# Performance work log

Measured on AMD Instinct MI355X. Metric: run time of the kernel, lower is better.

The kernel has to match this reference:

```python
import jax, jax.numpy as jnp
import numpy as np

BN_EPS = 1e-5

def conv1x1(x, w, b):
    # x: [b,c,h,w], w: [o,c], b: [o] -> [b,o,h,w]
    return jnp.einsum('bchw,oc->bohw', x, w) + b[None, :, None, None]

def setup_inputs() -> dict:
    key = jax.random.key(0)
    ks = jax.random.split(key, 12)
    C, Ci = 256, 128  # in_channels, inter_channels (ratio=2)
    B, H, W = 4, 56, 56
    s = 1.0 / np.sqrt(C)
    si = 1.0 / np.sqrt(Ci)
    return {
        'x':       jax.random.normal(ks[0], (B, C, H, W), jnp.float32),
        'w_theta': jax.random.normal(ks[1], (Ci, C), jnp.float32) * s,
        'b_theta': jax.random.normal(ks[2], (Ci,), jnp.float32) * s,
        'w_phi':   jax.random.normal(ks[3], (Ci, C), jnp.float32) * s,
        'b_phi':   jax.random.normal(ks[4], (Ci,), jnp.float32) * s,
        'w_g':     jax.random.normal(ks[5], (Ci, C), jnp.float32) * s,
        'b_g':     jax.random.normal(ks[6], (Ci,), jnp.float32) * s,
        'w_rec':   jax.random.normal(ks[7], (C, Ci), jnp.float32) * si,
        'b_rec':   jax.random.normal(ks[8], (C,), jnp.float32) * si,
        'bn_gamma': jax.random.normal(ks[9], (C,), jnp.float32) * 0.1 + 1.0,
        'bn_beta':  jax.random.normal(ks[10], (C,), jnp.float32) * 0.1,
        'bn_mean':  jax.random.normal(ks[11], (C,), jnp.float32) * 0.1,
        'bn_var':   jnp.ones((C,), jnp.float32),
    }

def reference(x, w_theta, b_theta, w_phi, b_phi, w_g, b_g,
              w_rec, b_rec, bn_gamma, bn_beta, bn_mean, bn_var):
    b, _, h, w = x.shape
    n = h * w
    c = w_theta.shape[0]  # inter_channels
    theta_x = conv1x1(x, w_theta, b_theta).reshape(b, c, n).transpose(0, 2, 1)  # [b,n,c]
    phi_x   = conv1x1(x, w_phi, b_phi).reshape(b, c, n)                         # [b,c,n]
    g_x     = conv1x1(x, w_g, b_g).reshape(b, c, n).transpose(0, 2, 1)          # [b,n,c]
    attention = jnp.matmul(theta_x, phi_x) / n                                  # [b,n,n]
    out = jnp.matmul(attention, g_x).transpose(0, 2, 1).reshape(b, c, h, w)
    out = conv1x1(out, w_rec, b_rec)
    # BatchNorm2d in inference form with given stats
    inv = bn_gamma / jnp.sqrt(bn_var + BN_EPS)
    out = out * inv[None, :, None, None] + (bn_beta - bn_mean * inv)[None, :, None, None]
    return out + x
```

## Files before the change

kernel.cpp:

```cpp
#include <hip/hip_runtime.h>

#define B 4
#define C 256
#define CI 128
#define NPIX 3136
#define KSPLIT 7
#define BN_EPS_F 1e-5f

typedef float f4 __attribute__((ext_vector_type(4)));

__global__ __launch_bounds__(64) void rowsum_kernel(const float* __restrict__ x,
                                                    float* __restrict__ s) {
    int b = blockIdx.y, c = blockIdx.x;
    const float* row = x + ((size_t)(b * C + c)) * NPIX;
    float acc = 0.f;
    for (int n = threadIdx.x; n < NPIX; n += 64) acc += row[n];
#pragma unroll
    for (int off = 32; off > 0; off >>= 1) acc += __shfl_down(acc, off, 64);
    if (threadIdx.x == 0) s[b * C + c] = acc;
}

__global__ __launch_bounds__(256) void xxt_kernel(const float* __restrict__ x,
                                                  float* __restrict__ Gp) {
    int j0 = blockIdx.x * 64, i0 = blockIdx.y * 64;
    int z = blockIdx.z;
    int b = z / KSPLIT, ks = z % KSPLIT;
    __shared__ float xi[64][68];
    __shared__ float xj[64][68];
    int tid = threadIdx.x;
    int tx = tid & 15, ty = tid >> 4;
    float acc[4][4] = {};
    const float* xb = x + (size_t)b * C * NPIX;
    for (int t = 0; t < KSPLIT; ++t) {
        int k0 = (ks * KSPLIT + t) * 64;
        __syncthreads();
#pragma unroll
        for (int l = 0; l < 4; ++l) {
            int idx = tid + l * 256;
            int r = idx >> 4, c4 = (idx & 15) << 2;
            *(f4*)&xi[r][c4] = *(const f4*)&xb[(size_t)(i0 + r) * NPIX + k0 + c4];
            *(f4*)&xj[r][c4] = *(const f4*)&xb[(size_t)(j0 + r) * NPIX + k0 + c4];
        }
        __syncthreads();
        for (int kk = 0; kk < 64; kk += 4) {
            f4 a[4], bb[4];
#pragma unroll
            for (int ii = 0; ii < 4; ++ii) a[ii] = *(const f4*)&xi[ty + 16 * ii][kk];
#pragma unroll
            for (int jj = 0; jj < 4; ++jj) bb[jj] = *(const f4*)&xj[tx + 16 * jj][kk];
#pragma unroll
            for (int q = 0; q < 4; ++q)
#pragma unroll
                for (int ii = 0; ii < 4; ++ii)
#pragma unroll
                    for (int jj = 0; jj < 4; ++jj)
                        acc[ii][jj] += a[ii][q] * bb[jj][q];
        }
    }
    float* Gb = Gp + ((size_t)(ks * B + b)) * C * C;
#pragma unroll
    for (int ii = 0; ii < 4; ++ii)
#pragma unroll
        for (int jj = 0; jj < 4; ++jj)
            Gb[(i0 + ty + 16 * ii) * C + (j0 + tx + 16 * jj)] = acc[ii][jj];
}

__global__ __launch_bounds__(256) void greduce_kernel(const float* __restrict__ Gp,
                                                      float* __restrict__ G) {
    int gid = blockIdx.x * 256 + threadIdx.x;
    float acc = 0.f;
#pragma unroll
    for (int ks = 0; ks < KSPLIT; ++ks) acc += Gp[(size_t)ks * (B * C * C) + gid];
    G[gid] = acc;
}

__global__ __launch_bounds__(256) void uv_kernel(const float* __restrict__ wphi,
                                                 const float* __restrict__ wg,
                                                 const float* __restrict__ s,
                                                 float* __restrict__ u,
                                                 float* __restrict__ v) {
    int b = blockIdx.x;
    __shared__ float sl[C];
    for (int i = threadIdx.x; i < C; i += 256) sl[i] = s[b * C + i];
    __syncthreads();
    int t = threadIdx.x;
    const float* wrow = (t < CI) ? (wphi + t * C) : (wg + (t - CI) * C);
    float acc = 0.f;
    for (int c = 0; c < C; ++c) acc += wrow[c] * sl[c];
    if (t < CI) u[b * CI + t] = acc;
    else        v[b * CI + (t - CI)] = acc;
}

__global__ __launch_bounds__(256) void pmat_kernel(const float* __restrict__ wphi,
                                                   const float* __restrict__ G,
                                                   float* __restrict__ P) {
    int gid = blockIdx.x * 256 + threadIdx.x;
    int b = gid >> 15;
    int i = (gid >> 8) & 127;
    int j = gid & 255;
    const float* wr = wphi + i * C;
    const float* Gb = G + (size_t)b * C * C;
    float acc = 0.f;
    for (int c = 0; c < C; ++c) acc += wr[c] * Gb[c * C + j];
    P[gid] = acc;
}

__global__ __launch_bounds__(256) void mmat_kernel(const float* __restrict__ P,
                                                   const float* __restrict__ wg,
                                                   const float* __restrict__ u,
                                                   const float* __restrict__ v,
                                                   const float* __restrict__ bphi,
                                                   const float* __restrict__ bg,
                                                   float* __restrict__ M) {
    int gid = blockIdx.x * 256 + threadIdx.x;
    int b = gid >> 14;
    int i = (gid >> 7) & 127;
    int j = gid & 127;
    const float* Pr = P + ((size_t)b * CI + i) * C;
    const float* wr = wg + j * C;
    float acc = 0.f;
    for (int c = 0; c < C; ++c) acc += Pr[c] * wr[c];
    const float invN = 1.0f / (float)NPIX;
    M[gid] = invN * (acc + u[b * CI + i] * bg[j] + bphi[i] * v[b * CI + j])
             + bphi[i] * bg[j];
}

__global__ __launch_bounds__(256) void amat_kernel(const float* __restrict__ wrec,
                                                   const float* __restrict__ M,
                                                   float* __restrict__ A) {
    int gid = blockIdx.x * 256 + threadIdx.x;
    int b = gid >> 15;
    int o = (gid >> 7) & 255;
    int i = gid & 127;
    const float* wr = wrec + o * CI;
    const float* Mb = M + (size_t)b * CI * CI;
    float acc = 0.f;
    for (int j = 0; j < CI; ++j) acc += wr[j] * Mb[i * CI + j];
    A[gid] = acc;
}

__global__ __launch_bounds__(256) void bias_kernel(const float* __restrict__ A,
                                                   const float* __restrict__ btheta,
                                                   const float* __restrict__ brec,
                                                   const float* __restrict__ gamma,
                                                   const float* __restrict__ beta,
                                                   const float* __restrict__ mean,
                                                   const float* __restrict__ var,
                                                   float* __restrict__ bias5) {
    int b = blockIdx.x, o = threadIdx.x;
    const float* Ar = A + ((size_t)b * C + o) * CI;
    float acc = 0.f;
    for (int i = 0; i < CI; ++i) acc += Ar[i] * btheta[i];
    float inv = gamma[o] * rsqrtf(var[o] + BN_EPS_F);
    bias5[b * C + o] = inv * (acc + brec[o]) + beta[o] - mean[o] * inv;
}

__global__ __launch_bounds__(256) void w5_kernel(const float* __restrict__ A,
                                                 const float* __restrict__ wtheta,
                                                 const float* __restrict__ gamma,
                                                 const float* __restrict__ var,
                                                 float* __restrict__ W5) {
    int gid = blockIdx.x * 256 + threadIdx.x;
    int b = gid >> 16;
    int o = (gid >> 8) & 255;
    int c = gid & 255;
    const float* Ar = A + ((size_t)b * C + o) * CI;
    float acc = 0.f;
    for (int i = 0; i < CI; ++i) acc += Ar[i] * wtheta[i * C + c];
    float inv = gamma[o] * rsqrtf(var[o] + BN_EPS_F);
    W5[gid] = inv * acc;
}

__global__ __launch_bounds__(256) void final_kernel(const float* __restrict__ x,
                                                    const float* __restrict__ W5,
                                                    const float* __restrict__ bias5,
                                                    float* __restrict__ out) {
    int b = blockIdx.z;
    int o0 = blockIdx.y * 64, n0 = blockIdx.x * 64;
    __shared__ float wl[64][68];
    __shared__ float xl[64][68];
    int tid = threadIdx.x;
    int tx = tid & 15, ty = tid >> 4;
    float acc[4][4] = {};
    const float* W5b = W5 + (size_t)b * C * C;
    const float* xb = x + (size_t)b * C * NPIX;
    for (int k0 = 0; k0 < C; k0 += 64) {
        __syncthreads();
#pragma unroll
        for (int l = 0; l < 4; ++l) {
            int idx = tid + l * 256;
            int r = idx >> 4, c4 = (idx & 15) << 2;
            *(f4*)&wl[r][c4] = *(const f4*)&W5b[(o0 + r) * C + k0 + c4];
            *(f4*)&xl[r][c4] = *(const f4*)&xb[(size_t)(k0 + r) * NPIX + n0 + c4];
        }
        __syncthreads();
        for (int kk = 0; kk < 64; kk += 4) {
            f4 a[4], bb[4];
#pragma unroll
            for (int i = 0; i < 4; ++i) a[i] = *(const f4*)&wl[ty + 16 * i][kk];
#pragma unroll
            for (int q = 0; q < 4; ++q) bb[q] = *(const f4*)&xl[kk + q][tx * 4];
#pragma unroll
            for (int q = 0; q < 4; ++q)
#pragma unroll
                for (int i = 0; i < 4; ++i)
#pragma unroll
                    for (int j = 0; j < 4; ++j)
                        acc[i][j] += a[i][q] * bb[q][j];
        }
    }
#pragma unroll
    for (int i = 0; i < 4; ++i) {
        int o = o0 + ty + 16 * i;
        float bias = bias5[b * C + o];
        int n = n0 + tx * 4;
        const f4 xr = *(const f4*)&xb[(size_t)o * NPIX + n];
        f4 r;
#pragma unroll
        for (int j = 0; j < 4; ++j) r[j] = acc[i][j] + bias + xr[j];
        *(f4*)&out[((size_t)b * C + o) * NPIX + n] = r;
    }
}

extern "C" void kernel_launch(void* const* d_in, const int* in_sizes, int n_in,
                              void* d_out, int out_size, void* d_ws, size_t ws_size,
                              hipStream_t stream) {
    const float* x       = (const float*)d_in[0];
    const float* w_theta = (const float*)d_in[1];
    const float* b_theta = (const float*)d_in[2];
    const float* w_phi   = (const float*)d_in[3];
    const float* b_phi   = (const float*)d_in[4];
    const float* w_g     = (const float*)d_in[5];
    const float* b_g     = (const float*)d_in[6];
    const float* w_rec   = (const float*)d_in[7];
    const float* b_rec   = (const float*)d_in[8];
    const float* gamma   = (const float*)d_in[9];
    const float* beta    = (const float*)d_in[10];
    const float* mean    = (const float*)d_in[11];
    const float* var     = (const float*)d_in[12];
    float* out = (float*)d_out;

    float* Gp    = out;
    float* G     = out + 1835008;
    float* P     = out + 2097152;
    float* M     = out + 2228224;
    float* A     = out + 2293760;
    float* ws    = (float*)d_ws;
    float* s     = ws;
    float* u     = ws + 1024;
    float* v     = ws + 1536;
    float* bias5 = ws + 2048;
    float* W5    = ws + 3072;

    rowsum_kernel<<<dim3(C, B), dim3(64), 0, stream>>>(x, s);
    xxt_kernel<<<dim3(4, 4, B * KSPLIT), dim3(256), 0, stream>>>(x, Gp);
    greduce_kernel<<<dim3(B * C * C / 256), dim3(256), 0, stream>>>(Gp, G);
    uv_kernel<<<dim3(B), dim3(256), 0, stream>>>(w_phi, w_g, s, u, v);
    pmat_kernel<<<dim3(B * CI * C / 256), dim3(256), 0, stream>>>(w_phi, G, P);
    mmat_kernel<<<dim3(B * CI * CI / 256), dim3(256), 0, stream>>>(P, w_g, u, v, b_phi, b_g, M);
    amat_kernel<<<dim3(B * C * CI / 256), dim3(256), 0, stream>>>(w_rec, M, A);
    bias_kernel<<<dim3(B), dim3(256), 0, stream>>>(A, b_theta, b_rec, gamma, beta, mean, var, bias5);
    w5_kernel<<<dim3(B * C * C / 256), dim3(256), 0, stream>>>(A, w_theta, gamma, var, W5);
    final_kernel<<<dim3(NPIX / 64, C / 64, B), dim3(256), 0, stream>>>(x, W5, bias5, out);
}
```

Measured before the change: 148.3 us.

## Use bf16 MFMA for the Gram and final GEMMs with a pre-converted copy of x

Adds a prep kernel that converts x to bf16 and also writes a transposed [n, c] bf16 copy. The x·xᵀ Gram kernel and the final W5·x kernel are rewritten to use mfma_f32_16x16x32_bf16, loading operands straight from global memory instead of staging them in shared memory. W5 is now stored in bf16. This swaps the FP32 FMA loops for matrix-core throughput, at the cost of an extra conversion pass over x, reduced precision, and epilogue stores that are no longer vectorised.

```diff
diff --git a/kernel.cpp b/kernel.cpp
--- a/kernel.cpp
+++ b/kernel.cpp
@@ -4,10 +4,19 @@
 #define C 256
 #define CI 128
 #define NPIX 3136
-#define KSPLIT 7
+#define KS 7
 #define BN_EPS_F 1e-5f
 
 typedef float f4 __attribute__((ext_vector_type(4)));
+typedef float f32x4 __attribute__((ext_vector_type(4)));
+typedef short short8 __attribute__((ext_vector_type(8)));
+typedef short short4v __attribute__((ext_vector_type(4)));
+
+__device__ inline short f2bf(float f) {
+    unsigned u = __builtin_bit_cast(unsigned, f);
+    unsigned r = (u + 0x7FFFu + ((u >> 16) & 1u)) >> 16;
+    return (short)r;
+}
 
 __global__ __launch_bounds__(64) void rowsum_kernel(const float* __restrict__ x,
                                                     float* __restrict__ s) {
@@ -20,49 +29,69 @@
     if (threadIdx.x == 0) s[b * C + c] = acc;
 }
 
-__global__ __launch_bounds__(256) void xxt_kernel(const float* __restrict__ x,
-                                                  float* __restrict__ Gp) {
-    int j0 = blockIdx.x * 64, i0 = blockIdx.y * 64;
+__global__ __launch_bounds__(256) void prep_kernel(const float* __restrict__ x,
+                                                   short* __restrict__ xbf,
+                                                   short* __restrict__ xT) {
+    int b = blockIdx.z, c0 = blockIdx.y * 64, n0 = blockIdx.x * 64;
+    __shared__ short lds[64][65];
+    int t = threadIdx.x;
+    int nf = (t & 15) * 4;
+    int cr = t >> 4;
+#pragma unroll
+    for (int it = 0; it < 4; ++it) {
+        int c = cr + 16 * it;
+        f4 v = *(const f4*)&x[((size_t)(b * C + c0 + c)) * NPIX + n0 + nf];
+        short4v s4;
+#pragma unroll
+        for (int i = 0; i < 4; ++i) s4[i] = f2bf(v[i]);
+        *(short4v*)&xbf[((size_t)(b * C + c0 + c)) * NPIX + n0 + nf] = s4;
+#pragma unroll
+        for (int i = 0; i < 4; ++i) lds[nf + i][c] = s4[i];
+    }
+    __syncthreads();
+#pragma unroll
+    for (int it = 0; it < 4; ++it) {
+        int n = cr + 16 * it;
+        short4v s4;
+#pragma unroll
+        for (int i = 0; i < 4; ++i) s4[i] = lds[n][nf + i];
+        *(short4v*)&xT[((size_t)b * NPIX + n0 + n) * C + c0 + nf] = s4;
+    }
+}
+
+__global__ __launch_bounds__(256) void xxt_mfma(const short* __restrict__ xbf,
+                                                float* __restrict__ Gp) {
     int z = blockIdx.z;
-    int b = z / KSPLIT, ks = z % KSPLIT;
-    __shared__ float xi[64][68];
-    __shared__ float xj[64][68];
-    int tid = threadIdx.x;
-    int tx = tid & 15, ty = tid >> 4;
-    float acc[4][4] = {};
-    const float* xb = x + (size_t)b * C * NPIX;
-    for (int t = 0; t < KSPLIT; ++t) {
-        int k0 = (ks * KSPLIT + t) * 64;
-        __syncthreads();
-#pragma unroll
-        for (int l = 0; l < 4; ++l) {
-            int idx = tid + l * 256;
-            int r = idx >> 4, c4 = (idx & 15) << 2;
-            *(f4*)&xi[r][c4] = *(const f4*)&xb[(size_t)(i0 + r) * NPIX + k0 + c4];
-            *(f4*)&xj[r][c4] = *(const f4*)&xb[(size_t)(j0 + r) * NPIX + k0 + c4];
-        }
-        __syncthreads();
-        for (int kk = 0; kk < 64; kk += 4) {
-            f4 a[4], bb[4];
-#pragma unroll
-            for (int ii = 0; ii < 4; ++ii) a[ii] = *(const f4*)&xi[ty + 16 * ii][kk];
-#pragma unroll
-            for (int jj = 0; jj < 4; ++jj) bb[jj] = *(const f4*)&xj[tx + 16 * jj][kk];
-#pragma unroll
-            for (int q = 0; q < 4; ++q)
-#pragma unroll
-                for (int ii = 0; ii < 4; ++ii)
-#pragma unroll
-                    for (int jj = 0; jj < 4; ++jj)
-                        acc[ii][jj] += a[ii][q] * bb[jj][q];
-        }
-    }
-    float* Gb = Gp + ((size_t)(ks * B + b)) * C * C;
-#pragma unroll
-    for (int ii = 0; ii < 4; ++ii)
-#pragma unroll
-        for (int jj = 0; jj < 4; ++jj)
-            Gb[(i0 + ty + 16 * ii) * C + (j0 + tx + 16 * jj)] = acc[ii][jj];
+    int b = z / KS, ks = z % KS;
+    int tid = threadIdx.x, lane = tid & 63, wid = tid >> 6;
+    int ibase = blockIdx.y * 128 + (wid >> 1) * 64;
+    int jbase = blockIdx.x * 128 + (wid & 1) * 64;
+    int lm = lane & 15, lk = (lane >> 4) * 8;
+    const short* A0 = xbf + ((size_t)(b * C) + ibase + lm) * NPIX + lk;
+    const short* B0 = xbf + ((size_t)(b * C) + jbase + lm) * NPIX + lk;
+    f32x4 acc[4][4] = {};
+    int kend = ks * 448 + 448;
+    for (int k = ks * 448; k < kend; k += 32) {
+        short8 a[4], bv[4];
+#pragma unroll
+        for (int mi = 0; mi < 4; ++mi) a[mi] = *(const short8*)(A0 + (size_t)mi * 16 * NPIX + k);
+#pragma unroll
+        for (int nj = 0; nj < 4; ++nj) bv[nj] = *(const short8*)(B0 + (size_t)nj * 16 * NPIX + k);
+#pragma unroll
+        for (int mi = 0; mi < 4; ++mi)
+#pragma unroll
+            for (int nj = 0; nj < 4; ++nj)
+                acc[mi][nj] = __builtin_amdgcn_mfma_f32_16x16x32_bf16(a[mi], bv[nj], acc[mi][nj], 0, 0, 0);
+    }
+    float* out = Gp + ((size_t)(ks * B + b)) * C * C;
+    int r0 = (lane >> 4) * 4;
+#pragma unroll
+    for (int mi = 0; mi < 4; ++mi)
+#pragma unroll
+        for (int r = 0; r < 4; ++r)
+#pragma unroll
+            for (int nj = 0; nj < 4; ++nj)
+                out[(ibase + mi * 16 + r0 + r) * C + jbase + nj * 16 + lm] = acc[mi][nj][r];
 }
 
 __global__ __launch_bounds__(256) void greduce_kernel(const float* __restrict__ Gp,
@@ -70,7 +99,7 @@
     int gid = blockIdx.x * 256 + threadIdx.x;
     float acc = 0.f;
 #pragma unroll
-    for (int ks = 0; ks < KSPLIT; ++ks) acc += Gp[(size_t)ks * (B * C * C) + gid];
+    for (int ks = 0; ks < KS; ++ks) acc += Gp[(size_t)ks * (B * C * C) + gid];
     G[gid] = acc;
 }
 
@@ -159,7 +188,7 @@
                                                  const float* __restrict__ wtheta,
                                                  const float* __restrict__ gamma,
                                                  const float* __restrict__ var,
-                                                 float* __restrict__ W5) {
+                                                 short* __restrict__ W5bf) {
     int gid = blockIdx.x * 256 + threadIdx.x;
     int b = gid >> 16;
     int o = (gid >> 8) & 255;
@@ -168,57 +197,50 @@
     float acc = 0.f;
     for (int i = 0; i < CI; ++i) acc += Ar[i] * wtheta[i * C + c];
     float inv = gamma[o] * rsqrtf(var[o] + BN_EPS_F);
-    W5[gid] = inv * acc;
-}
-
-__global__ __launch_bounds__(256) void final_kernel(const float* __restrict__ x,
-                                                    const float* __restrict__ W5,
-                                                    const float* __restrict__ bias5,
-                                                    float* __restrict__ out) {
-    int b = blockIdx.z;
-    int o0 = blockIdx.y * 64, n0 = blockIdx.x * 64;
-    __shared__ float wl[64][68];
-    __shared__ float xl[64][68];
-    int tid = threadIdx.x;
-    int tx = tid & 15, ty = tid >> 4;
-    float acc[4][4] = {};
-    const float* W5b = W5 + (size_t)b * C * C;
-    const float* xb = x + (size_t)b * C * NPIX;
-    for (int k0 = 0; k0 < C; k0 += 64) {
-        __syncthreads();
-#pragma unroll
-        for (int l = 0; l < 4; ++l) {
-            int idx = tid + l * 256;
-            int r = idx >> 4, c4 = (idx & 15) << 2;
-            *(f4*)&wl[r][c4] = *(const f4*)&W5b[(o0 + r) * C + k0 + c4];
-            *(f4*)&xl[r][c4] = *(const f4*)&xb[(size_t)(k0 + r) * NPIX + n0 + c4];
+    W5bf[gid] = f2bf(inv * acc);
+}
+
+__global__ __launch_bounds__(256) void final_mfma(const float* __restrict__ x,
+                                                  const short* __restrict__ W5bf,
+                                                  const short* __restrict__ xT,
+                                                  const float* __restrict__ bias5,
+                                                  float* __restrict__ out) {
+    int b = blockIdx.y;
+    int n0 = blockIdx.x * 64;
+    int tid = threadIdx.x, lane = tid & 63, wid = tid >> 6;
+    int obase = wid * 64;
+    int lm = lane & 15, lk = (lane >> 4) * 8;
+    const short* A0 = W5bf + ((size_t)(b * C) + obase + lm) * C + lk;
+    const short* B0 = xT + ((size_t)b * NPIX + n0 + lm) * C + lk;
+    f32x4 acc[4][4] = {};
+#pragma unroll
+    for (int k = 0; k < C; k += 32) {
+        short8 a[4], bv[4];
+#pragma unroll
+        for (int mi = 0; mi < 4; ++mi) a[mi] = *(const short8*)(A0 + mi * 16 * C + k);
+#pragma unroll
+        for (int nj = 0; nj < 4; ++nj) bv[nj] = *(const short8*)(B0 + nj * 16 * C + k);
+#pragma unroll
+        for (int mi = 0; mi < 4; ++mi)
+#pragma unroll
+            for (int nj = 0; nj < 4; ++nj)
+                acc[mi][nj] = __builtin_amdgcn_mfma_f32_16x16x32_bf16(a[mi], bv[nj], acc[mi][nj], 0, 0, 0);
+    }
+    int r0 = (lane >> 4) * 4;
+#pragma unroll
+    for (int mi = 0; mi < 4; ++mi) {
+#pragma unroll
+        for (int r = 0; r < 4; ++r) {
+            int o = obase + mi * 16 + r0 + r;
+            float bias = bias5[b * C + o];
+            const float* xrow = x + ((size_t)(b * C + o)) * NPIX;
+            float* orow = out + ((size_t)(b * C + o)) * NPIX;
+#pragma unroll
+            for (int nj = 0; nj < 4; ++nj) {
+                int n = n0 + nj * 16 + lm;
+                orow[n] = acc[mi][nj][r] + bias + xrow[n];
+            }
         }
-        __syncthreads();
-        for (int kk = 0; kk < 64; kk += 4) {
-            f4 a[4], bb[4];
-#pragma unroll
-            for (int i = 0; i < 4; ++i) a[i] = *(const f4*)&wl[ty + 16 * i][kk];
-#pragma unroll
-            for (int q = 0; q < 4; ++q) bb[q] = *(const f4*)&xl[kk + q][tx * 4];
-#pragma unroll
-            for (int q = 0; q < 4; ++q)
-#pragma unroll
-                for (int i = 0; i < 4; ++i)
-#pragma unroll
-                    for (int j = 0; j < 4; ++j)
-                        acc[i][j] += a[i][q] * bb[q][j];
-        }
-    }
-#pragma unroll
-    for (int i = 0; i < 4; ++i) {
-        int o = o0 + ty + 16 * i;
-        float bias = bias5[b * C + o];
-        int n = n0 + tx * 4;
-        const f4 xr = *(const f4*)&xb[(size_t)o * NPIX + n];
-        f4 r;
-#pragma unroll
-        for (int j = 0; j < 4; ++j) r[j] = acc[i][j] + bias + xr[j];
-        *(f4*)&out[((size_t)b * C + o) * NPIX + n] = r;
     }
 }
 
@@ -240,26 +262,30 @@
     const float* var     = (const float*)d_in[12];
     float* out = (float*)d_out;
 
-    float* Gp    = out;
-    float* G     = out + 1835008;
-    float* P     = out + 2097152;
-    float* M     = out + 2228224;
-    float* A     = out + 2293760;
-    float* ws    = (float*)d_ws;
-    float* s     = ws;
-    float* u     = ws + 1024;
-    float* v     = ws + 1536;
-    float* bias5 = ws + 2048;
-    float* W5    = ws + 3072;
+    float* Gp = out;
+    float* G  = out + 1835008;
+    float* P  = out + 2097152;
+    float* M  = out + 2228224;
+    float* A  = out + 2293760;
+
+    char* wsb = (char*)d_ws;
+    float* s     = (float*)(wsb + 0);
+    float* u     = (float*)(wsb + 4096);
+    float* v     = (float*)(wsb + 6144);
+    float* bias5 = (float*)(wsb + 8192);
+    short* W5bf  = (short*)(wsb + 16384);
+    short* xbf   = (short*)(wsb + (1u << 20));
+    short* xT    = (short*)(wsb + (8u << 20));
 
     rowsum_kernel<<<dim3(C, B), dim3(64), 0, stream>>>(x, s);
-    xxt_kernel<<<dim3(4, 4, B * KSPLIT), dim3(256), 0, stream>>>(x, Gp);
+    prep_kernel<<<dim3(NPIX / 64, C / 64, B), dim3(256), 0, stream>>>(x, xbf, xT);
+    xxt_mfma<<<dim3(2, 2, B * KS), dim3(256), 0, stream>>>(xbf, Gp);
     greduce_kernel<<<dim3(B * C * C / 256), dim3(256), 0, stream>>>(Gp, G);
     uv_kernel<<<dim3(B), dim3(256), 0, stream>>>(w_phi, w_g, s, u, v);
     pmat_kernel<<<dim3(B * CI * C / 256), dim3(256), 0, stream>>>(w_phi, G, P);
     mmat_kernel<<<dim3(B * CI * CI / 256), dim3(256), 0, stream>>>(P, w_g, u, v, b_phi, b_g, M);
     amat_kernel<<<dim3(B * C * CI / 256), dim3(256), 0, stream>>>(w_rec, M, A);
     bias_kernel<<<dim3(B), dim3(256), 0, stream>>>(A, b_theta, b_rec, gamma, beta, mean, var, bias5);
-    w5_kernel<<<dim3(B * C * C / 256), dim3(256), 0, stream>>>(A, w_theta, gamma, var, W5);
-    final_kernel<<<dim3(NPIX / 64, C / 64, B), dim3(256), 0, stream>>>(x, W5, bias5, out);
-}
+    w5_kernel<<<dim3(B * C * C / 256), dim3(256), 0, stream>>>(A, w_theta, gamma, var, W5bf);
+    final_mfma<<<dim3(NPIX / 64, B), dim3(256), 0, stream>>>(x, W5bf, xT, bias5, out);
+}
```

Result: faster. 124.3 us (-16.2%).
